# Performance work log

Measured on AMD Instinct MI355X. Metric: run time of the kernel, lower is better.

## Reference

```python
import jax, jax.numpy as jnp
import numpy as np
import math

EMBED_DIM = 1024
NUM_HEADS = 16
HEAD_DIM = EMBED_DIM // NUM_HEADS
MAX_SEQ_LEN = 1024
B, L = 4, 1024


def _sinusoidal_rel_emb(max_seq_len, dim):
    # positions -(max_seq_len-1) .. (max_seq_len-1), sinusoidal init as in torch module
    positions = np.arange(-(max_seq_len - 1), max_seq_len, dtype=np.float32)[:, None]
    div_term = np.exp(np.arange(0, dim, 2, dtype=np.float32) * (-math.log(10000.0) / dim))
    emb = np.zeros((2 * max_seq_len - 1, dim), dtype=np.float32)
    emb[:, 0::2] = np.sin(positions * div_term)
    emb[:, 1::2] = np.cos(positions * div_term)
    return jnp.asarray(emb)


def setup_inputs() -> dict:
    key = jax.random.key(0)
    ks = jax.random.split(key, 12)
    s = 0.02
    return {
        "query": jax.random.normal(ks[0], (B, L, EMBED_DIM), jnp.float32),
        "key": jax.random.normal(ks[1], (B, L, EMBED_DIM), jnp.float32),
        "value": jax.random.normal(ks[2], (B, L, EMBED_DIM), jnp.float32),
        "mask": jnp.zeros((B, 1, L, L), dtype=bool),
        "Wq": jax.random.normal(ks[3], (EMBED_DIM, EMBED_DIM), jnp.float32) * s,
        "bq": jnp.zeros((EMBED_DIM,), jnp.float32),
        "Wk": jax.random.normal(ks[4], (EMBED_DIM, EMBED_DIM), jnp.float32) * s,
        "bk": jnp.zeros((EMBED_DIM,), jnp.float32),
        "Wv": jax.random.normal(ks[5], (EMBED_DIM, EMBED_DIM), jnp.float32) * s,
        "bv": jnp.zeros((EMBED_DIM,), jnp.float32),
        "Wo": jax.random.normal(ks[6], (EMBED_DIM, EMBED_DIM), jnp.float32) * s,
        "bo": jnp.zeros((EMBED_DIM,), jnp.float32),
        "rel_emb": _sinusoidal_rel_emb(MAX_SEQ_LEN, HEAD_DIM),  # [2*max-1, head_dim]
        "Wp": jax.random.normal(ks[7], (HEAD_DIM, HEAD_DIM), jnp.float32) * s,
    }


def _attn(query, key, value, mask, Wq, bq, Wk, bk, Wv, bv, Wo, bo, rel_emb, Wp):
    Bsz, Lq, E = query.shape
    Lk = key.shape[1]
    H, D = NUM_HEADS, HEAD_DIM
    scale = 1.0 / math.sqrt(D)

    Q = (query @ Wq.T + bq).reshape(Bsz, Lq, H, D).transpose(0, 2, 1, 3)  # [B,H,Lq,D]
    K = (key @ Wk.T + bk).reshape(Bsz, Lk, H, D).transpose(0, 2, 1, 3)
    V = (value @ Wv.T + bv).reshape(Bsz, Lk, H, D).transpose(0, 2, 1, 3)

    # relative embeddings for length Lk: rows for positions -(Lk-1)..(Lk-1)
    start = MAX_SEQ_LEN - Lk
    R = jax.lax.dynamic_slice_in_dim(rel_emb, start, 2 * Lk - 1, axis=0)  # [2Lk-1, D]
    Rk = R @ Wp.T  # pos_key_proj (no bias)

    content = jnp.einsum("bhqd,bhkd->bhqk", Q, K) * scale
    pos = jnp.einsum("bhqd,rd->bhqr", Q, Rk) * scale  # [B,H,Lq,2Lk-1]

    # rel_shift: out[i,j] = pos[i, j - i + Lk - 1]  (rel pos j-i)
    idx = jnp.arange(Lk)[None, :] - jnp.arange(Lq)[:, None] + (Lk - 1)  # [Lq,Lk]
    rel_scores = jnp.take_along_axis(pos, idx[None, None, :, :], axis=-1)

    scores = content + rel_scores
    scores = jnp.where(mask, -jnp.inf, scores)
    probs = jax.nn.softmax(scores, axis=-1)
    ctx = jnp.einsum("bhqk,bhkd->bhqd", probs, V)
    ctx = ctx.transpose(0, 2, 1, 3).reshape(Bsz, Lq, E)
    return ctx @ Wo.T + bo


def reference(query, key, value, mask, Wq, bq, Wk, bk, Wv, bv, Wo, bo, rel_emb, Wp):
    return _attn(query, key, value, mask, Wq, bq, Wk, bk, Wv, bv, Wo, bo, rel_emb, Wp)
```

## Files before the change

### kernel.cpp

```cpp
#include <hip/hip_runtime.h>
#include <stdint.h>

#define SEQ 1024
#define EMBED 1024
#define NH 16
#define HD 64

typedef unsigned short u16;
typedef __attribute__((ext_vector_type(8))) short s16x8;
typedef __attribute__((ext_vector_type(4))) float f32x4;

__device__ __forceinline__ float bf2f(u16 h) {
  union { uint32_t u; float f; } x; x.u = ((uint32_t)h) << 16; return x.f;
}
__device__ __forceinline__ u16 f2bf(float f) {
  union { float f; uint32_t u; } x; x.f = f;
  uint32_t u = x.u;
  return (u16)((u + 0x7fffu + ((u >> 16) & 1u)) >> 16);
}
__device__ __forceinline__ f32x4 mfma16(s16x8 a, s16x8 b, f32x4 c) {
  return __builtin_amdgcn_mfma_f32_16x16x32_bf16(a, b, c, 0, 0, 0);
}

__global__ void detect_dtype(const u16* __restrict__ q, int* __restrict__ flag) {
  int lane = threadIdx.x;
  bool big = false;
  #pragma unroll
  for (int i = 0; i < 8; ++i) {
    float v = bf2f(q[lane * 8 + i]);
    if (!(fabsf(v) < 1024.0f)) big = true;
  }
  unsigned long long m = __ballot(big);
  if (lane == 0) *flag = (m != 0ULL) ? 1 : 0;
}

struct CastJobs { const void* src[13]; u16* dst[13]; int n[13]; };

__global__ void cast_all(CastJobs J, const int* __restrict__ flag) {
  int j = blockIdx.y;
  int base = (blockIdx.x * 256 + threadIdx.x) * 8;
  if (base >= J.n[j]) return;
  u16* dst = J.dst[j] + base;
  if (*flag) {
    const float* s = (const float*)J.src[j] + base;
    float4 a = *(const float4*)s;
    float4 b = *(const float4*)(s + 4);
    u16 t[8] = {f2bf(a.x), f2bf(a.y), f2bf(a.z), f2bf(a.w),
                f2bf(b.x), f2bf(b.y), f2bf(b.z), f2bf(b.w)};
    *(uint4*)dst = *(const uint4*)t;
  } else {
    *(uint4*)dst = *(const uint4*)((const u16*)J.src[j] + base);
  }
}

__device__ __forceinline__ void stage8(u16* dst, const void* src, size_t elt,
                                       bool f32) {
  if (f32) {
    const float* s = (const float*)src + elt;
    float4 x0 = *(const float4*)s;
    float4 x1 = *(const float4*)(s + 4);
    u16 t[8] = {f2bf(x0.x), f2bf(x0.y), f2bf(x0.z), f2bf(x0.w),
                f2bf(x1.x), f2bf(x1.y), f2bf(x1.z), f2bf(x1.w)};
    *(uint4*)dst = *(const uint4*)t;
  } else {
    *(uint4*)dst = *(const uint4*)((const u16*)src + elt);
  }
}

template <int TM, bool PURE>
__global__ __launch_bounds__(256, 2) void gemm_bt(
    const void* __restrict__ A0, const void* __restrict__ A1,
    const void* __restrict__ A2, const void* __restrict__ B0,
    const void* __restrict__ B1, const void* __restrict__ B2,
    const u16* __restrict__ bias0, const u16* __restrict__ bias1,
    const u16* __restrict__ bias2, void* __restrict__ C0,
    void* __restrict__ C1, void* __restrict__ C2, u16* __restrict__ VT,
    int M, int N, int K, const int* __restrict__ flag,
    int aMode, int bMode, int cMode, int vtMode)
{
  constexpr int MB = TM / 32;
  constexpr int SMU = (TM == 128) ? 16640 : (TM * 64 + 128 * 64);
  __shared__ u16 smem[SMU];
  u16* As = smem;
  u16* Bs = smem + TM * 64;

  const int z = blockIdx.z;
  const void* A = z == 0 ? A0 : z == 1 ? A1 : A2;
  const void* B = z == 0 ? B0 : z == 1 ? B1 : B2;
  const u16* bias = z == 0 ? bias0 : z == 1 ? bias1 : bias2;
  void* C = z == 0 ? C0 : z == 1 ? C1 : C2;

  const bool f32 = (*flag != 0);
  const bool aF = PURE ? false : (aMode && f32);
  const bool bF = PURE ? false : (bMode && f32);
  const bool cF = cMode && f32;
  const bool doVT = vtMode && (z == 2);

  const int tid = threadIdx.x;
  const int lane = tid & 63;
  const int w = tid >> 6;
  const int wr = w >> 1, wc = w & 1;
  const int l15 = lane & 15, l4 = lane >> 4;
  const int q7 = l15 & 7;
  const int m0 = blockIdx.x * TM, n0 = blockIdx.y * 128;

  f32x4 acc[MB][4] = {};

  for (int k0 = 0; k0 < K; k0 += 64) {
    #pragma unroll
    for (int i = 0; i < MB; ++i) {
      int c = tid + 256 * i;
      int r = c >> 3, m = c & 7;
      stage8(&As[r * 64 + (m ^ (r & 7)) * 8], A,
             (size_t)(m0 + r) * K + k0 + m * 8, aF);
    }
    #pragma unroll
    for (int i = 0; i < 4; ++i) {
      int c = tid + 256 * i;
      int r = c >> 3, m = c & 7;
      stage8(&Bs[r * 64 + (m ^ (r & 7)) * 8], B,
             (size_t)(n0 + r) * K + k0 + m * 8, bF);
    }
    __syncthreads();
    #pragma unroll
    for (int kc = 0; kc < 2; ++kc) {
      s16x8 af[MB], bfr[4];
      #pragma unroll
      for (int mb = 0; mb < MB; ++mb)
        af[mb] = *(const s16x8*)&As[(wr * (TM / 2) + mb * 16 + l15) * 64 +
                                    8 * ((kc * 4 + l4) ^ q7)];
      #pragma unroll
      for (int nb = 0; nb < 4; ++nb)
        bfr[nb] = *(const s16x8*)&Bs[(wc * 64 + nb * 16 + l15) * 64 +
                                     8 * ((kc * 4 + l4) ^ q7)];
      #pragma unroll
      for (int mb = 0; mb < MB; ++mb)
        #pragma unroll
        for (int nb = 0; nb < 4; ++nb)
          acc[mb][nb] = mfma16(af[mb], bfr[nb], acc[mb][nb]);
    }
    __syncthreads();
  }

  if (doVT) {
    u16* Ts = smem;
    #pragma unroll
    for (int nb = 0; nb < 4; ++nb) {
      int nl = wc * 64 + nb * 16 + l15;
      float bv = bf2f(bias[n0 + nl]);
      #pragma unroll
      for (int mb = 0; mb < MB; ++mb)
        #pragma unroll
        for (int r = 0; r < 4; ++r) {
          int ml = wr * (TM / 2) + mb * 16 + l4 * 4 + r;
          Ts[ml * 130 + nl] = f2bf(acc[mb][nb][r] + bv);
        }
    }
    __syncthreads();
    int n = tid & 127, mh = tid >> 7;
    int gcol = n0 + n;
    int hh = gcol >> 6, dd = gcol & 63;
    int bb = m0 >> 10;
    size_t gbase = ((size_t)(bb * NH + hh) * HD + dd) * SEQ +
                   (m0 & (SEQ - 1)) + mh * 64;
    #pragma unroll
    for (int t = 0; t < 8; ++t) {
      union { u16 h[8]; uint4 v; } tmp;
      #pragma unroll
      for (int j = 0; j < 8; ++j) tmp.h[j] = Ts[(mh * 64 + t * 8 + j) * 130 + n];
      *(uint4*)&VT[gbase + t * 8] = tmp.v;
    }
  } else {
    #pragma unroll
    for (int nb = 0; nb < 4; ++nb) {
      int col = n0 + wc * 64 + nb * 16 + l15;
      float bv = bf2f(bias[col]);
      #pragma unroll
      for (int mb = 0; mb < MB; ++mb) {
        int rbase = m0 + wr * (TM / 2) + mb * 16 + l4 * 4;
        #pragma unroll
        for (int r = 0; r < 4; ++r) {
          float v = acc[mb][nb][r] + bv;
          if (cF) ((float*)C)[(size_t)(rbase + r) * N + col] = v;
          else    ((u16*)C)[(size_t)(rbase + r) * N + col] = f2bf(v);
        }
      }
    }
  }
}

__global__ void rk_proj(const u16* __restrict__ relb, const u16* __restrict__ Wpb,
                        u16* __restrict__ Rk)
{
  int idx = blockIdx.x * 256 + threadIdx.x;
  int r = idx >> 6, d = idx & 63;
  float s = 0.f;
  if (r < 2047) {
    #pragma unroll 8
    for (int j = 0; j < 64; ++j)
      s += bf2f(relb[r * 64 + j]) * bf2f(Wpb[d * 64 + j]);
  }
  Rk[idx] = f2bf(s);
}

__global__ __launch_bounds__(256, 3) void attn_kernel(
    const u16* Qp, const u16* __restrict__ Kp,
    const u16* __restrict__ VT, const u16* __restrict__ Rk,
    u16* ctx)
{
  __shared__ u16 Qs[64 * 64];
  __shared__ u16 Ks[64 * 64];
  __shared__ u16 Vts[64 * 64];
  __shared__ u16 Rs[128 * 64];
  __shared__ u16 Ps[4][16 * 64];

  const int tid = threadIdx.x;
  const int lane = tid & 63;
  const int w = tid >> 6;
  const int l15 = lane & 15, l4 = lane >> 4;
  const int q7 = l15 & 7;
  const int qt = blockIdx.x;
  const int bh = blockIdx.y;
  const int b = bh >> 4, h = bh & 15;
  const int q0 = qt * 64;

  #pragma unroll
  for (int i = 0; i < 2; ++i) {
    int c = tid + 256 * i;
    int r = c >> 3, m = c & 7;
    *(uint4*)&Qs[r * 64 + (m ^ (r & 7)) * 8] =
        *(const uint4*)&Qp[(size_t)(b * SEQ + q0 + r) * EMBED + h * HD + m * 8];
  }
  __syncthreads();
  s16x8 aq0 = *(const s16x8*)&Qs[(w * 16 + l15) * 64 + 8 * (l4 ^ q7)];
  s16x8 aq1 = *(const s16x8*)&Qs[(w * 16 + l15) * 64 + 8 * ((4 + l4) ^ q7)];

  float lsum[4] = {0.f, 0.f, 0.f, 0.f};
  f32x4 o[4];
  #pragma unroll
  for (int d = 0; d < 4; ++d) o[d] = (f32x4){0.f, 0.f, 0.f, 0.f};

  for (int kt = 0; kt < 16; ++kt) {
    const int k0 = kt * 64;
    __syncthreads();
    #pragma unroll
    for (int i = 0; i < 2; ++i) {
      int c = tid + 256 * i;
      int r = c >> 3, m = c & 7;
      *(uint4*)&Ks[r * 64 + (m ^ (r & 7)) * 8] =
          *(const uint4*)&Kp[(size_t)(b * SEQ + k0 + r) * EMBED + h * HD + m * 8];
      *(uint4*)&Vts[r * 64 + (m ^ (r & 7)) * 8] =
          *(const uint4*)&VT[((size_t)(b * NH + h) * HD + r) * SEQ + k0 + m * 8];
    }
    const int rbase = k0 - q0 + 960;
    #pragma unroll
    for (int i = 0; i < 4; ++i) {
      int c = tid + 256 * i;
      int r = c >> 3, m = c & 7;
      *(uint4*)&Rs[r * 64 + (m ^ (r & 7)) * 8] =
          *(const uint4*)&Rk[(size_t)(rbase + r) * HD + m * 8];
    }
    __syncthreads();

    f32x4 sacc[4];
    #pragma unroll
    for (int nb = 0; nb < 4; ++nb) {
      s16x8 b0 = *(const s16x8*)&Ks[(nb * 16 + l15) * 64 + 8 * (l4 ^ q7)];
      s16x8 b1 = *(const s16x8*)&Ks[(nb * 16 + l15) * 64 + 8 * ((4 + l4) ^ q7)];
      f32x4 t = {};
      t = mfma16(aq0, b0, t);
      t = mfma16(aq1, b1, t);
      sacc[nb] = t;
    }

    const int rowoff = 48 - 16 * w;
    f32x4 rt[5];
    #pragma unroll
    for (int nb = 0; nb < 5; ++nb) {
      s16x8 b0 = *(const s16x8*)&Rs[(rowoff + nb * 16 + l15) * 64 + 8 * (l4 ^ q7)];
      s16x8 b1 = *(const s16x8*)&Rs[(rowoff + nb * 16 + l15) * 64 + 8 * ((4 + l4) ^ q7)];
      f32x4 t = {};
      t = mfma16(aq0, b0, t);
      t = mfma16(aq1, b1, t);
      rt[nb] = t;
    }

    #pragma unroll
    for (int r = 0; r < 4; ++r) {
      int qi = l4 * 4 + r;
      int delta = l15 + 15 - qi;
      int srcLane = l4 * 16 + (delta & 15);
      float sh[5];
      #pragma unroll
      for (int nb = 0; nb < 5; ++nb) sh[nb] = __shfl(rt[nb][r], srcLane, 64);
      #pragma unroll
      for (int nb = 0; nb < 4; ++nb) {
        float relv = (delta < 16) ? sh[nb] : sh[nb + 1];
        float p = __expf((sacc[nb][r] + relv) * 0.125f);
        lsum[r] += p;
        int ch = (nb * 2 + (l15 >> 3)) ^ (qi & 7);
        Ps[w][qi * 64 + ch * 8 + q7] = f2bf(p);
      }
    }

    asm volatile("s_waitcnt lgkmcnt(0)" ::: "memory");

    s16x8 ap0 = *(const s16x8*)&Ps[w][l15 * 64 + 8 * (l4 ^ q7)];
    s16x8 ap1 = *(const s16x8*)&Ps[w][l15 * 64 + 8 * ((4 + l4) ^ q7)];

    #pragma unroll
    for (int d = 0; d < 4; ++d) {
      s16x8 b0 = *(const s16x8*)&Vts[(d * 16 + l15) * 64 + 8 * (l4 ^ q7)];
      s16x8 b1 = *(const s16x8*)&Vts[(d * 16 + l15) * 64 + 8 * ((4 + l4) ^ q7)];
      o[d] = mfma16(ap0, b0, o[d]);
      o[d] = mfma16(ap1, b1, o[d]);
    }
  }

  float inv[4];
  #pragma unroll
  for (int r = 0; r < 4; ++r) {
    float rs = lsum[r];
    #pragma unroll
    for (int off = 1; off < 16; off <<= 1)
      rs += __shfl_xor(rs, off, 64);
    inv[r] = 1.0f / rs;
  }

  #pragma unroll
  for (int d = 0; d < 4; ++d) {
    int col = h * HD + d * 16 + l15;
    #pragma unroll
    for (int r = 0; r < 4; ++r) {
      int row = b * SEQ + q0 + w * 16 + l4 * 4 + r;
      ctx[(size_t)row * EMBED + col] = f2bf(o[d][r] * inv[r]);
    }
  }
}

extern "C" void kernel_launch(void* const* d_in, const int* in_sizes, int n_in,
                              void* d_out, int out_size, void* d_ws, size_t ws_size,
                              hipStream_t stream) {
  const void* q   = d_in[0];
  const void* k   = d_in[1];
  const void* v   = d_in[2];
  const void* Wq  = d_in[4];
  const void* bq  = d_in[5];
  const void* Wk  = d_in[6];
  const void* bk  = d_in[7];
  const void* Wv  = d_in[8];
  const void* bv  = d_in[9];
  const void* Wo  = d_in[10];
  const void* bo  = d_in[11];
  const void* rel = d_in[12];
  const void* Wp  = d_in[13];

  char* p = (char*)d_ws;
  int* flag = (int*)p;               p += 256;
  u16* Rk   = (u16*)p;               p += (size_t)2048 * 64 * 2;
  u16* relb = (u16*)p;               p += (size_t)262144;
  u16* Wpb  = (u16*)p;               p += 8192;
  u16* bqb  = (u16*)p;               p += 2048;
  u16* bkb  = (u16*)p;               p += 2048;
  u16* bvb  = (u16*)p;               p += 2048;
  u16* bob  = (u16*)p;               p += 2048;
  u16* Qp   = (u16*)p;               p += (size_t)4096 * 1024 * 2;
  u16* Kp   = (u16*)p;               p += (size_t)4096 * 1024 * 2;
  u16* Wqb  = (u16*)p;               p += (size_t)1024 * 1024 * 2;
  u16* Wkb  = (u16*)p;               p += (size_t)1024 * 1024 * 2;
  u16* Wvb  = (u16*)p;               p += (size_t)1024 * 1024 * 2;
  u16* Wob  = (u16*)p;               p += (size_t)1024 * 1024 * 2;
  u16* qb   = (u16*)p;               p += (size_t)4096 * 1024 * 2;
  u16* kb   = (u16*)p;               p += (size_t)4096 * 1024 * 2;
  u16* vb   = (u16*)p;               p += (size_t)4096 * 1024 * 2;
  size_t need_primary = (size_t)(p - (char*)d_ws);
  const bool primary = ws_size >= need_primary;

  u16* VT = (u16*)d_out;
  u16* cx = Qp;

  dim3 blk(256);
  detect_dtype<<<1, 64, 0, stream>>>((const u16*)q, flag);

  CastJobs J = {};
  J.src[0] = bq;  J.dst[0] = bqb;  J.n[0] = 1024;
  J.src[1] = bk;  J.dst[1] = bkb;  J.n[1] = 1024;
  J.src[2] = bv;  J.dst[2] = bvb;  J.n[2] = 1024;
  J.src[3] = bo;  J.dst[3] = bob;  J.n[3] = 1024;
  J.src[4] = rel; J.dst[4] = relb; J.n[4] = 2047 * 64;
  J.src[5] = Wp;  J.dst[5] = Wpb;  J.n[5] = 64 * 64;
  if (primary) {
    J.src[6]  = Wq; J.dst[6]  = Wqb; J.n[6]  = 1024 * 1024;
    J.src[7]  = Wk; J.dst[7]  = Wkb; J.n[7]  = 1024 * 1024;
    J.src[8]  = Wv; J.dst[8]  = Wvb; J.n[8]  = 1024 * 1024;
    J.src[9]  = Wo; J.dst[9]  = Wob; J.n[9]  = 1024 * 1024;
    J.src[10] = q;  J.dst[10] = qb;  J.n[10] = 4096 * 1024;
    J.src[11] = k;  J.dst[11] = kb;  J.n[11] = 4096 * 1024;
    J.src[12] = v;  J.dst[12] = vb;  J.n[12] = 4096 * 1024;
    cast_all<<<dim3(2048, 13), blk, 0, stream>>>(J, flag);
    gemm_bt<128, true><<<dim3(32, 8, 3), blk, 0, stream>>>(
        qb, kb, vb, Wqb, Wkb, Wvb, bqb, bkb, bvb,
        Qp, Kp, nullptr, VT, 4096, 1024, 1024, flag, 0, 0, 0, 1);
  } else {
    cast_all<<<dim3(64, 6), blk, 0, stream>>>(J, flag);
    gemm_bt<128, false><<<dim3(32, 8, 3), blk, 0, stream>>>(
        q, k, v, Wq, Wk, Wv, bqb, bkb, bvb,
        Qp, Kp, nullptr, VT, 4096, 1024, 1024, flag, 1, 1, 0, 1);
  }
  rk_proj<<<512, blk, 0, stream>>>(relb, Wpb, Rk);
  attn_kernel<<<dim3(16, 64), blk, 0, stream>>>(Qp, Kp, VT, Rk, cx);
  if (primary) {
    gemm_bt<64, true><<<dim3(64, 8, 1), blk, 0, stream>>>(
        cx, cx, cx, Wob, Wob, Wob, bob, bob, bob,
        d_out, d_out, d_out, nullptr, 4096, 1024, 1024, flag, 0, 0, 1, 0);
  } else {
    gemm_bt<64, false><<<dim3(64, 8, 1), blk, 0, stream>>>(
        cx, cx, cx, Wo, Wo, Wo, bob, bob, bob,
        d_out, d_out, d_out, nullptr, 4096, 1024, 1024, flag, 0, 1, 1, 0);
  }
}
```

Baseline: 310.0 us.

## Prefetch K/V/R tiles into registers and reuse R halves via ring buffer

The attention kernel now issues global loads for the next K, V^T and relative-embedding tiles into registers before computing the current tile, so load latency overlaps with the MFMA work. The 128-row R window is split into two 64-row halves in a two-slot ring, so only one new half is loaded per iteration instead of all 128 rows. Separately, the GEMM kernel uses direct global-to-LDS loads (global_load_lds) on the pure-bf16 path and drops the XOR swizzle from its shared tiles. Dropping the swizzle may bring back LDS bank conflicts on fragment reads, and the register prefetch raises register pressure under launch_bounds(256,3).

```diff
diff --git a/kernel.cpp b/kernel.cpp
--- a/kernel.cpp
+++ b/kernel.cpp
@@ -20,6 +20,12 @@
 }
 __device__ __forceinline__ f32x4 mfma16(s16x8 a, s16x8 b, f32x4 c) {
   return __builtin_amdgcn_mfma_f32_16x16x32_bf16(a, b, c, 0, 0, 0);
+}
+
+__device__ __forceinline__ void gll16(const u16* g, u16* l) {
+  auto gp = (const __attribute__((address_space(1))) void*)(uintptr_t)g;
+  auto lp = (__attribute__((address_space(3))) void*)(uintptr_t)l;
+  __builtin_amdgcn_global_load_lds(gp, lp, 16, 0, 0);
 }
 
 __global__ void detect_dtype(const u16* __restrict__ q, int* __restrict__ flag) {
@@ -101,25 +107,37 @@
   const int w = tid >> 6;
   const int wr = w >> 1, wc = w & 1;
   const int l15 = lane & 15, l4 = lane >> 4;
-  const int q7 = l15 & 7;
   const int m0 = blockIdx.x * TM, n0 = blockIdx.y * 128;
 
   f32x4 acc[MB][4] = {};
 
   for (int k0 = 0; k0 < K; k0 += 64) {
-    #pragma unroll
-    for (int i = 0; i < MB; ++i) {
-      int c = tid + 256 * i;
-      int r = c >> 3, m = c & 7;
-      stage8(&As[r * 64 + (m ^ (r & 7)) * 8], A,
-             (size_t)(m0 + r) * K + k0 + m * 8, aF);
-    }
-    #pragma unroll
-    for (int i = 0; i < 4; ++i) {
-      int c = tid + 256 * i;
-      int r = c >> 3, m = c & 7;
-      stage8(&Bs[r * 64 + (m ^ (r & 7)) * 8], B,
-             (size_t)(n0 + r) * K + k0 + m * 8, bF);
+    if (PURE) {
+      #pragma unroll
+      for (int i = 0; i < MB; ++i) {
+        int c = tid + 256 * i;
+        int r = c >> 3, m = c & 7;
+        gll16(&((const u16*)A)[(size_t)(m0 + r) * K + k0 + m * 8], &As[c * 8]);
+      }
+      #pragma unroll
+      for (int i = 0; i < 4; ++i) {
+        int c = tid + 256 * i;
+        int r = c >> 3, m = c & 7;
+        gll16(&((const u16*)B)[(size_t)(n0 + r) * K + k0 + m * 8], &Bs[c * 8]);
+      }
+    } else {
+      #pragma unroll
+      for (int i = 0; i < MB; ++i) {
+        int c = tid + 256 * i;
+        int r = c >> 3, m = c & 7;
+        stage8(&As[c * 8], A, (size_t)(m0 + r) * K + k0 + m * 8, aF);
+      }
+      #pragma unroll
+      for (int i = 0; i < 4; ++i) {
+        int c = tid + 256 * i;
+        int r = c >> 3, m = c & 7;
+        stage8(&Bs[c * 8], B, (size_t)(n0 + r) * K + k0 + m * 8, bF);
+      }
     }
     __syncthreads();
     #pragma unroll
@@ -128,11 +146,11 @@
       #pragma unroll
       for (int mb = 0; mb < MB; ++mb)
         af[mb] = *(const s16x8*)&As[(wr * (TM / 2) + mb * 16 + l15) * 64 +
-                                    8 * ((kc * 4 + l4) ^ q7)];
+                                    kc * 32 + l4 * 8];
       #pragma unroll
       for (int nb = 0; nb < 4; ++nb)
         bfr[nb] = *(const s16x8*)&Bs[(wc * 64 + nb * 16 + l15) * 64 +
-                                     8 * ((kc * 4 + l4) ^ q7)];
+                                     kc * 32 + l4 * 8];
       #pragma unroll
       for (int mb = 0; mb < MB; ++mb)
         #pragma unroll
@@ -211,7 +229,7 @@
   __shared__ u16 Qs[64 * 64];
   __shared__ u16 Ks[64 * 64];
   __shared__ u16 Vts[64 * 64];
-  __shared__ u16 Rs[128 * 64];
+  __shared__ u16 Rs[2][64 * 64];
   __shared__ u16 Ps[4][16 * 64];
 
   const int tid = threadIdx.x;
@@ -223,14 +241,27 @@
   const int bh = blockIdx.y;
   const int b = bh >> 4, h = bh & 15;
   const int q0 = qt * 64;
-
-  #pragma unroll
-  for (int i = 0; i < 2; ++i) {
-    int c = tid + 256 * i;
-    int r = c >> 3, m = c & 7;
-    *(uint4*)&Qs[r * 64 + (m ^ (r & 7)) * 8] =
-        *(const uint4*)&Qp[(size_t)(b * SEQ + q0 + r) * EMBED + h * HD + m * 8];
-  }
+  const int g0row = 960 - q0;
+
+  const int c0 = tid, c1 = tid + 256;
+  const int r0 = c0 >> 3, mm0 = c0 & 7;
+  const int r1 = c1 >> 3, mm1 = c1 & 7;
+  const int sw0 = (mm0 ^ (r0 & 7)) * 8;
+  const int sw1 = (mm1 ^ (r1 & 7)) * 8;
+  const size_t kvb = (size_t)(b * SEQ) * EMBED + h * HD;
+  const size_t vtb = (size_t)(b * NH + h) * HD * SEQ;
+
+  uint4 pk0 = *(const uint4*)&Kp[kvb + (size_t)r0 * EMBED + mm0 * 8];
+  uint4 pk1 = *(const uint4*)&Kp[kvb + (size_t)r1 * EMBED + mm1 * 8];
+  uint4 pv0 = *(const uint4*)&VT[vtb + (size_t)r0 * SEQ + mm0 * 8];
+  uint4 pv1 = *(const uint4*)&VT[vtb + (size_t)r1 * SEQ + mm1 * 8];
+  uint4 pr0 = *(const uint4*)&Rk[(size_t)(g0row + r0) * HD + mm0 * 8];
+  uint4 pr1 = *(const uint4*)&Rk[(size_t)(g0row + r1) * HD + mm1 * 8];
+  uint4 pr2 = *(const uint4*)&Rk[(size_t)(g0row + 64 + r0) * HD + mm0 * 8];
+  uint4 pr3 = *(const uint4*)&Rk[(size_t)(g0row + 64 + r1) * HD + mm1 * 8];
+
+  *(uint4*)&Qs[r0 * 64 + sw0] = *(const uint4*)&Qp[kvb + (size_t)(q0 + r0) * EMBED + mm0 * 8];
+  *(uint4*)&Qs[r1 * 64 + sw1] = *(const uint4*)&Qp[kvb + (size_t)(q0 + r1) * EMBED + mm1 * 8];
   __syncthreads();
   s16x8 aq0 = *(const s16x8*)&Qs[(w * 16 + l15) * 64 + 8 * (l4 ^ q7)];
   s16x8 aq1 = *(const s16x8*)&Qs[(w * 16 + l15) * 64 + 8 * ((4 + l4) ^ q7)];
@@ -240,27 +271,36 @@
   #pragma unroll
   for (int d = 0; d < 4; ++d) o[d] = (f32x4){0.f, 0.f, 0.f, 0.f};
 
+  const int rowoff = 48 - 16 * w;
+
   for (int kt = 0; kt < 16; ++kt) {
-    const int k0 = kt * 64;
+    if (kt) __syncthreads();
+    *(uint4*)&Ks[r0 * 64 + sw0] = pk0;
+    *(uint4*)&Ks[r1 * 64 + sw1] = pk1;
+    *(uint4*)&Vts[r0 * 64 + sw0] = pv0;
+    *(uint4*)&Vts[r1 * 64 + sw1] = pv1;
+    if (kt == 0) {
+      *(uint4*)&Rs[0][r0 * 64 + sw0] = pr0;
+      *(uint4*)&Rs[0][r1 * 64 + sw1] = pr1;
+      *(uint4*)&Rs[1][r0 * 64 + sw0] = pr2;
+      *(uint4*)&Rs[1][r1 * 64 + sw1] = pr3;
+    } else {
+      const int s = (kt + 1) & 1;
+      *(uint4*)&Rs[s][r0 * 64 + sw0] = pr0;
+      *(uint4*)&Rs[s][r1 * 64 + sw1] = pr1;
+    }
     __syncthreads();
-    #pragma unroll
-    for (int i = 0; i < 2; ++i) {
-      int c = tid + 256 * i;
-      int r = c >> 3, m = c & 7;
-      *(uint4*)&Ks[r * 64 + (m ^ (r & 7)) * 8] =
-          *(const uint4*)&Kp[(size_t)(b * SEQ + k0 + r) * EMBED + h * HD + m * 8];
-      *(uint4*)&Vts[r * 64 + (m ^ (r & 7)) * 8] =
-          *(const uint4*)&VT[((size_t)(b * NH + h) * HD + r) * SEQ + k0 + m * 8];
-    }
-    const int rbase = k0 - q0 + 960;
-    #pragma unroll
-    for (int i = 0; i < 4; ++i) {
-      int c = tid + 256 * i;
-      int r = c >> 3, m = c & 7;
-      *(uint4*)&Rs[r * 64 + (m ^ (r & 7)) * 8] =
-          *(const uint4*)&Rk[(size_t)(rbase + r) * HD + m * 8];
-    }
-    __syncthreads();
+
+    if (kt < 15) {
+      const int k0n = (kt + 1) * 64;
+      pk0 = *(const uint4*)&Kp[kvb + (size_t)(k0n + r0) * EMBED + mm0 * 8];
+      pk1 = *(const uint4*)&Kp[kvb + (size_t)(k0n + r1) * EMBED + mm1 * 8];
+      pv0 = *(const uint4*)&VT[vtb + (size_t)r0 * SEQ + k0n + mm0 * 8];
+      pv1 = *(const uint4*)&VT[vtb + (size_t)r1 * SEQ + k0n + mm1 * 8];
+      const int gr = g0row + (kt + 2) * 64;
+      pr0 = *(const uint4*)&Rk[(size_t)(gr + r0) * HD + mm0 * 8];
+      pr1 = *(const uint4*)&Rk[(size_t)(gr + r1) * HD + mm1 * 8];
+    }
 
     f32x4 sacc[4];
     #pragma unroll
@@ -273,12 +313,14 @@
       sacc[nb] = t;
     }
 
-    const int rowoff = 48 - 16 * w;
     f32x4 rt[5];
     #pragma unroll
     for (int nb = 0; nb < 5; ++nb) {
-      s16x8 b0 = *(const s16x8*)&Rs[(rowoff + nb * 16 + l15) * 64 + 8 * (l4 ^ q7)];
-      s16x8 b1 = *(const s16x8*)&Rs[(rowoff + nb * 16 + l15) * 64 + 8 * ((4 + l4) ^ q7)];
+      const int bl = rowoff + nb * 16;
+      const int s = (kt + (bl >> 6)) & 1;
+      const int rr = (bl & 63) + l15;
+      s16x8 b0 = *(const s16x8*)&Rs[s][rr * 64 + 8 * (l4 ^ q7)];
+      s16x8 b1 = *(const s16x8*)&Rs[s][rr * 64 + 8 * ((4 + l4) ^ q7)];
       f32x4 t = {};
       t = mfma16(aq0, b0, t);
       t = mfma16(aq1, b1, t);
```

Result: slower. 323.5 us (+4.3%).
